# Optimization experiments

Hardware: AMD Instinct MI355X
Metric: run time of the kernel (lower is better)

The kernel has to match this reference:

```python
import jax, jax.numpy as jnp
import numpy as np

E, C, O = 500_000, 64, 64

def setup_inputs() -> dict:
    key = jax.random.key(0)
    k1, k2, k3, k4 = jax.random.split(key, 4)
    x = jax.random.normal(k1, (E, C), dtype=jnp.float32)
    # neighbors in [-1, E): -1 marks a missing neighbor (boundary edge)
    neighbors = jax.random.randint(k2, (E, 4), -1, E, dtype=jnp.int32)
    # Linear(5C -> O): kaiming-ish init
    W = jax.random.normal(k3, (O, 5 * C), dtype=jnp.float32) * (1.0 / np.sqrt(5 * C))
    b = jax.random.normal(k4, (O,), dtype=jnp.float32) * 0.01
    return {"x": x, "neighbors": neighbors, "W": W, "b": b}

def reference(x, neighbors, W, b):
    E_, C_ = x.shape
    safe_nb = jnp.maximum(neighbors, 0)                      # clamp(min=0)
    nb_feats = x[safe_nb]                                    # [E, 4, C] gather
    missing = (neighbors < 0)[..., None]                     # [E, 4, 1]
    nb_feats = jnp.where(missing, jnp.zeros((), x.dtype), nb_feats)
    pair1 = jnp.sort(nb_feats[:, 0:2, :], axis=1)            # elementwise sort of 2
    pair2 = jnp.sort(nb_feats[:, 2:4, :], axis=1)
    combined = jnp.concatenate(
        [x, pair1.reshape(E_, 2 * C_), pair2.reshape(E_, 2 * C_)], axis=1
    )                                                         # [E, 5C]
    return combined @ W.T + b                                 # [E, O]
```

## Files before the change

kernel.cpp:

```cpp
#include <hip/hip_runtime.h>

#define E_TOT 500000
#define C_DIM 64

typedef __attribute__((ext_vector_type(8))) _Float16 half8;
typedef __attribute__((ext_vector_type(4))) float f32x4;

__global__ __launch_bounds__(256)
void cvt_x_kernel(const float* __restrict__ x, _Float16* __restrict__ x16) {
  const size_t i = (size_t)blockIdx.x * 256 + threadIdx.x;
  const float4* src = (const float4*)x + 2 * i;
  float4 u = src[0], v = src[1];
  half8 h;
  h[0] = (_Float16)u.x; h[1] = (_Float16)u.y; h[2] = (_Float16)u.z; h[3] = (_Float16)u.w;
  h[4] = (_Float16)v.x; h[5] = (_Float16)v.y; h[6] = (_Float16)v.z; h[7] = (_Float16)v.w;
  *((half8*)x16 + i) = h;
}

template <bool USE16>
__global__ __launch_bounds__(512, 4)
void meshconv_main(const float* __restrict__ x, const _Float16* __restrict__ x16,
                   const int* __restrict__ nbr, const float* __restrict__ W,
                   const float* __restrict__ bias, float* __restrict__ out) {
  __shared__ _Float16 Wh[20480];

  const int tid = threadIdx.x;
  for (int fidx = tid; fidx < 2560; fidx += 512) {
    const int l   = fidx & 63;
    const int t   = (fidx >> 6) & 3;
    const int ks  = fidx >> 8;
    const int row = t * 16 + (l & 15);
    const int col = ks * 32 + (l >> 4) * 8;
    const float* src = W + row * 320 + col;
    float4 u = *(const float4*)src;
    float4 v = *(const float4*)(src + 4);
    half8 h;
    h[0] = (_Float16)u.x; h[1] = (_Float16)u.y; h[2] = (_Float16)u.z; h[3] = (_Float16)u.w;
    h[4] = (_Float16)v.x; h[5] = (_Float16)v.y; h[6] = (_Float16)v.z; h[7] = (_Float16)v.w;
    *reinterpret_cast<half8*>(&Wh[fidx * 8]) = h;
  }
  __syncthreads();

  const int lane = tid & 63;
  const int wv   = tid >> 6;
  const int lrow = lane & 15;
  const int kc8  = (lane >> 4) * 8;

  const int base = blockIdx.x * 256 + wv * 32;
  const int e0  = base + lrow;
  const int e1  = base + 16 + lrow;
  const int ec0 = min(e0, E_TOT - 1);
  const int ec1 = min(e1, E_TOT - 1);

  const int4 nb0 = *(const int4*)(nbr + ec0 * 4);
  const int4 nb1 = *(const int4*)(nbr + ec1 * 4);

  f32x4 acc[2][4];
#pragma unroll
  for (int m = 0; m < 2; ++m)
#pragma unroll
    for (int t = 0; t < 4; ++t) acc[m][t] = (f32x4){0.f, 0.f, 0.f, 0.f};

  auto gat = [&](int row, int h) -> half8 {
    if constexpr (USE16) {
      return *reinterpret_cast<const half8*>(x16 + (size_t)row * 64 + h * 32 + kc8);
    } else {
      const float* p = x + (size_t)row * 64 + h * 32 + kc8;
      float4 u = *(const float4*)p;
      float4 v = *(const float4*)(p + 4);
      half8 r;
      r[0] = (_Float16)u.x; r[1] = (_Float16)u.y; r[2] = (_Float16)u.z; r[3] = (_Float16)u.w;
      r[4] = (_Float16)v.x; r[5] = (_Float16)v.y; r[6] = (_Float16)v.z; r[7] = (_Float16)v.w;
      return r;
    }
  };

  auto mnmx = [&](half8 a, half8 b, int na, int nb_, half8& mn, half8& mx) {
    const half8 zero = (half8)(_Float16)0.0f;
    if (na < 0)  a = zero;
    if (nb_ < 0) b = zero;
    mn = __builtin_elementwise_min(a, b);
    mx = __builtin_elementwise_max(a, b);
  };

  auto dot2 = [&](int ks, half8 a0, half8 a1) {
#pragma unroll
    for (int t = 0; t < 4; ++t) {
      half8 w = *reinterpret_cast<const half8*>(&Wh[((ks * 4 + t) * 64 + lane) * 8]);
      acc[0][t] = __builtin_amdgcn_mfma_f32_16x16x32_f16(a0, w, acc[0][t], 0, 0, 0);
      acc[1][t] = __builtin_amdgcn_mfma_f32_16x16x32_f16(a1, w, acc[1][t], 0, 0, 0);
    }
  };

  const int r0a = max(nb0.x, 0), r0b = max(nb0.y, 0);
  const int r1a = max(nb1.x, 0), r1b = max(nb1.y, 0);
  const int r0c = max(nb0.z, 0), r0d = max(nb0.w, 0);
  const int r1c = max(nb1.z, 0), r1d = max(nb1.w, 0);

  half8 o00 = gat(ec0, 0), o01 = gat(ec0, 1);
  half8 o10 = gat(ec1, 0), o11 = gat(ec1, 1);

  half8 a00 = gat(r0a, 0), b00 = gat(r0b, 0);
  half8 a10 = gat(r1a, 0), b10 = gat(r1b, 0);
  half8 a01 = gat(r0a, 1), b01 = gat(r0b, 1);
  half8 a11 = gat(r1a, 1), b11 = gat(r1b, 1);

  dot2(0, o00, o10);
  dot2(1, o01, o11);

  half8 c00 = gat(r0c, 0), d00 = gat(r0d, 0);
  half8 c10 = gat(r1c, 0), d10 = gat(r1d, 0);
  half8 c01 = gat(r0c, 1), d01 = gat(r0d, 1);
  half8 c11 = gat(r1c, 1), d11 = gat(r1d, 1);

  {
    half8 mn0, mx0, mn1, mx1;
    mnmx(a00, b00, nb0.x, nb0.y, mn0, mx0);
    mnmx(a10, b10, nb1.x, nb1.y, mn1, mx1);
    dot2(2, mn0, mn1);
    dot2(4, mx0, mx1);
    mnmx(a01, b01, nb0.x, nb0.y, mn0, mx0);
    mnmx(a11, b11, nb1.x, nb1.y, mn1, mx1);
    dot2(3, mn0, mn1);
    dot2(5, mx0, mx1);
  }

  {
    half8 mn0, mx0, mn1, mx1;
    mnmx(c00, d00, nb0.z, nb0.w, mn0, mx0);
    mnmx(c10, d10, nb1.z, nb1.w, mn1, mx1);
    dot2(6, mn0, mn1);
    dot2(8, mx0, mx1);
    mnmx(c01, d01, nb0.z, nb0.w, mn0, mx0);
    mnmx(c11, d11, nb1.z, nb1.w, mn1, mx1);
    dot2(7, mn0, mn1);
    dot2(9, mx0, mx1);
  }

  float bv[4];
#pragma unroll
  for (int t = 0; t < 4; ++t) bv[t] = bias[t * 16 + lrow];

  const int lgrp = lane >> 4;
#pragma unroll
  for (int m = 0; m < 2; ++m)
#pragma unroll
    for (int r = 0; r < 4; ++r) {
      const int e = base + m * 16 + lgrp * 4 + r;
      if (e < E_TOT) {
        float* po = out + (size_t)e * 64 + lrow;
        po[0]  = acc[m][0][r] + bv[0];
        po[16] = acc[m][1][r] + bv[1];
        po[32] = acc[m][2][r] + bv[2];
        po[48] = acc[m][3][r] + bv[3];
      }
    }
}

extern "C" void kernel_launch(void* const* d_in, const int* in_sizes, int n_in,
                              void* d_out, int out_size, void* d_ws, size_t ws_size,
                              hipStream_t stream) {
  const float* x   = (const float*)d_in[0];
  const int*   nbr = (const int*)d_in[1];
  const float* W   = (const float*)d_in[2];
  const float* b   = (const float*)d_in[3];
  float* out = (float*)d_out;

  const int mblocks = (E_TOT + 255) / 256;
  const size_t need = (size_t)E_TOT * C_DIM * sizeof(_Float16);

  if (ws_size >= need) {
    _Float16* x16 = (_Float16*)d_ws;
    const int cblocks = (E_TOT * C_DIM) / (256 * 8);
    hipLaunchKernelGGL(cvt_x_kernel, dim3(cblocks), dim3(256), 0, stream, x, x16);
    hipLaunchKernelGGL((meshconv_main<true>), dim3(mblocks), dim3(512), 0, stream,
                       x, x16, nbr, W, b, out);
  } else {
    hipLaunchKernelGGL((meshconv_main<false>), dim3(mblocks), dim3(512), 0, stream,
                       x, (const _Float16*)nullptr, nbr, W, b, out);
  }
}
```

Before: 298.2 us.

## Precompute fp16 W fragments once and transpose MFMA for vectorized output stores

The fp32-to-fp16 conversion and fragment swizzle of W moves into block 0 of the x conversion kernel. Each main block now just copies the prepared half8 fragments into shared memory instead of converting W itself. The MFMA operands are swapped so each lane holds four consecutive output columns of one edge. This lets the epilogue write float4 vector stores with vector bias adds instead of scalar strided stores. The cost is a serial tail in block 0 of the conversion kernel and a slightly larger workspace.

After: 291.8 us. 2.2% less time.

```diff
diff --git a/kernel.cpp b/kernel.cpp
--- a/kernel.cpp
+++ b/kernel.cpp
@@ -1,54 +1,62 @@
 #include <hip/hip_runtime.h>
 
 #define E_TOT 500000
-#define C_DIM 64
 
 typedef __attribute__((ext_vector_type(8))) _Float16 half8;
 typedef __attribute__((ext_vector_type(4))) float f32x4;
 
-__global__ __launch_bounds__(256)
-void cvt_x_kernel(const float* __restrict__ x, _Float16* __restrict__ x16) {
-  const size_t i = (size_t)blockIdx.x * 256 + threadIdx.x;
-  const float4* src = (const float4*)x + 2 * i;
-  float4 u = src[0], v = src[1];
+__device__ __forceinline__ half8 cvt8(float4 u, float4 v) {
   half8 h;
   h[0] = (_Float16)u.x; h[1] = (_Float16)u.y; h[2] = (_Float16)u.z; h[3] = (_Float16)u.w;
   h[4] = (_Float16)v.x; h[5] = (_Float16)v.y; h[6] = (_Float16)v.z; h[7] = (_Float16)v.w;
-  *((half8*)x16 + i) = h;
+  return h;
+}
+
+__global__ __launch_bounds__(256)
+void cvt_x_kernel(const float* __restrict__ x, const float* __restrict__ W,
+                  _Float16* __restrict__ x16, _Float16* __restrict__ Wfrag) {
+  const size_t i = (size_t)blockIdx.x * 256 + threadIdx.x;
+  const float4* src = (const float4*)x + 2 * i;
+  *((half8*)x16 + i) = cvt8(src[0], src[1]);
+  if (blockIdx.x == 0) {
+    for (int f = (int)threadIdx.x; f < 2560; f += 256) {
+      const int l = f & 63, t = (f >> 6) & 3, ks = f >> 8;
+      const float* s = W + (t * 16 + (l & 15)) * 320 + ks * 32 + (l >> 4) * 8;
+      *((half8*)Wfrag + f) = cvt8(*(const float4*)s, *(const float4*)(s + 4));
+    }
+  }
 }
 
 template <bool USE16>
 __global__ __launch_bounds__(512, 4)
 void meshconv_main(const float* __restrict__ x, const _Float16* __restrict__ x16,
-                   const int* __restrict__ nbr, const float* __restrict__ W,
-                   const float* __restrict__ bias, float* __restrict__ out) {
+                   const _Float16* __restrict__ Wfrag, const int* __restrict__ nbr,
+                   const float* __restrict__ W, const float* __restrict__ bias,
+                   float* __restrict__ out) {
   __shared__ _Float16 Wh[20480];
 
   const int tid = threadIdx.x;
-  for (int fidx = tid; fidx < 2560; fidx += 512) {
-    const int l   = fidx & 63;
-    const int t   = (fidx >> 6) & 3;
-    const int ks  = fidx >> 8;
-    const int row = t * 16 + (l & 15);
-    const int col = ks * 32 + (l >> 4) * 8;
-    const float* src = W + row * 320 + col;
-    float4 u = *(const float4*)src;
-    float4 v = *(const float4*)(src + 4);
-    half8 h;
-    h[0] = (_Float16)u.x; h[1] = (_Float16)u.y; h[2] = (_Float16)u.z; h[3] = (_Float16)u.w;
-    h[4] = (_Float16)v.x; h[5] = (_Float16)v.y; h[6] = (_Float16)v.z; h[7] = (_Float16)v.w;
-    *reinterpret_cast<half8*>(&Wh[fidx * 8]) = h;
+  if constexpr (USE16) {
+    for (int c = tid; c < 2560; c += 512)
+      *reinterpret_cast<half8*>(&Wh[c * 8]) = *((const half8*)Wfrag + c);
+  } else {
+    for (int f = tid; f < 2560; f += 512) {
+      const int l = f & 63, t = (f >> 6) & 3, ks = f >> 8;
+      const float* s = W + (t * 16 + (l & 15)) * 320 + ks * 32 + (l >> 4) * 8;
+      *reinterpret_cast<half8*>(&Wh[f * 8]) = cvt8(*(const float4*)s, *(const float4*)(s + 4));
+    }
   }
   __syncthreads();
 
   const int lane = tid & 63;
   const int wv   = tid >> 6;
-  const int lrow = lane & 15;
-  const int kc8  = (lane >> 4) * 8;
+  const int eoff = lane & 15;
+  const int g    = lane >> 4;
+  const int kc8  = g * 8;
 
   const int base = blockIdx.x * 256 + wv * 32;
-  const int e0  = base + lrow;
-  const int e1  = base + 16 + lrow;
+  const int e0  = base + eoff;
+  const int e1  = base + 16 + eoff;
   const int ec0 = min(e0, E_TOT - 1);
   const int ec1 = min(e1, E_TOT - 1);
 
@@ -66,12 +74,7 @@
       return *reinterpret_cast<const half8*>(x16 + (size_t)row * 64 + h * 32 + kc8);
     } else {
       const float* p = x + (size_t)row * 64 + h * 32 + kc8;
-      float4 u = *(const float4*)p;
-      float4 v = *(const float4*)(p + 4);
-      half8 r;
-      r[0] = (_Float16)u.x; r[1] = (_Float16)u.y; r[2] = (_Float16)u.z; r[3] = (_Float16)u.w;
-      r[4] = (_Float16)v.x; r[5] = (_Float16)v.y; r[6] = (_Float16)v.z; r[7] = (_Float16)v.w;
-      return r;
+      return cvt8(*(const float4*)p, *(const float4*)(p + 4));
     }
   };
 
@@ -87,8 +90,8 @@
 #pragma unroll
     for (int t = 0; t < 4; ++t) {
       half8 w = *reinterpret_cast<const half8*>(&Wh[((ks * 4 + t) * 64 + lane) * 8]);
-      acc[0][t] = __builtin_amdgcn_mfma_f32_16x16x32_f16(a0, w, acc[0][t], 0, 0, 0);
-      acc[1][t] = __builtin_amdgcn_mfma_f32_16x16x32_f16(a1, w, acc[1][t], 0, 0, 0);
+      acc[0][t] = __builtin_amdgcn_mfma_f32_16x16x32_f16(w, a0, acc[0][t], 0, 0, 0);
+      acc[1][t] = __builtin_amdgcn_mfma_f32_16x16x32_f16(w, a1, acc[1][t], 0, 0, 0);
     }
   };
 
@@ -137,24 +140,21 @@
     dot2(9, mx0, mx1);
   }
 
-  float bv[4];
+  f32x4 bv[4];
 #pragma unroll
-  for (int t = 0; t < 4; ++t) bv[t] = bias[t * 16 + lrow];
+  for (int t = 0; t < 4; ++t) bv[t] = *(const f32x4*)(bias + t * 16 + g * 4);
 
-  const int lgrp = lane >> 4;
 #pragma unroll
-  for (int m = 0; m < 2; ++m)
+  for (int m = 0; m < 2; ++m) {
+    const int e = base + m * 16 + eoff;
+    if (e < E_TOT) {
+      float* po = out + (size_t)e * 64 + g * 4;
 #pragma unroll
-    for (int r = 0; r < 4; ++r) {
-      const int e = base + m * 16 + lgrp * 4 + r;
-      if (e < E_TOT) {
-        float* po = out + (size_t)e * 64 + lrow;
-        po[0]  = acc[m][0][r] + bv[0];
-        po[16] = acc[m][1][r] + bv[1];
-        po[32] = acc[m][2][r] + bv[2];
-        po[48] = acc[m][3][r] + bv[3];
+      for (int t = 0; t < 4; ++t) {
+        *(f32x4*)(po + t * 16) = acc[m][t] + bv[t];
       }
     }
+  }
 }
 
 extern "C" void kernel_launch(void* const* d_in, const int* in_sizes, int n_in,
@@ -167,16 +167,20 @@
   float* out = (float*)d_out;
 
   const int mblocks = (E_TOT + 255) / 256;
-  const size_t need = (size_t)E_TOT * C_DIM * sizeof(_Float16);
+  const size_t x16_bytes = (size_t)E_TOT * 64 * sizeof(_Float16);
+  const size_t need = x16_bytes + 2560 * 8 * sizeof(_Float16);
 
   if (ws_size >= need) {
-    _Float16* x16 = (_Float16*)d_ws;
-    const int cblocks = (E_TOT * C_DIM) / (256 * 8);
-    hipLaunchKernelGGL(cvt_x_kernel, dim3(cblocks), dim3(256), 0, stream, x, x16);
+    _Float16* x16   = (_Float16*)d_ws;
+    _Float16* Wfrag = (_Float16*)((char*)d_ws + x16_bytes);
+    const int cblocks = (E_TOT * 64) / (256 * 8);
+    hipLaunchKernelGGL(cvt_x_kernel, dim3(cblocks), dim3(256), 0, stream,
+                       x, W, x16, Wfrag);
     hipLaunchKernelGGL((meshconv_main<true>), dim3(mblocks), dim3(512), 0, stream,
-                       x, x16, nbr, W, b, out);
+                       x, x16, Wfrag, nbr, W, b, out);
   } else {
     hipLaunchKernelGGL((meshconv_main<false>), dim3(mblocks), dim3(512), 0, stream,
-                       x, (const _Float16*)nullptr, nbr, W, b, out);
+                       x, (const _Float16*)nullptr, (const _Float16*)nullptr,
+                       nbr, W, b, out);
   }
 }
```
